# Optimization experiments

Measured on AMD Instinct MI355X. Metric: run time of the kernel, lower is better.

The kernel has to match this reference:

```python
import jax, jax.numpy as jnp
import numpy as np

N, E, D, B = 50000, 800000, 64, 64
NEXP, NC, EDIM, PDIM = 4, 10, 4, 100


def setup_inputs() -> dict:
    key = jax.random.key(0)
    ks = jax.random.split(key, 24)
    s = lambda f: 1.0 / np.sqrt(f)
    inp = {
        'x': jax.random.normal(ks[0], (N, D), jnp.float32),
        'edge_index': jax.random.randint(ks[1], (2, E), 0, N, jnp.int32),
        'edge_attr': jax.random.normal(ks[2], (E, EDIM), jnp.float32),
        'batch': jnp.sort(jax.random.randint(ks[3], (N,), 0, B, jnp.int32)),
        'ldxb_flag': jax.random.normal(ks[4], (B,), jnp.float32),
        # layer 1 params
        'w_edge1': jax.random.normal(ks[5], (D, EDIM)) * s(EDIM),
        'b_edge1': jnp.zeros((D,), jnp.float32),
        'w_ih1': jax.random.normal(ks[6], (3 * D, D)) * s(D),
        'w_hh1': jax.random.normal(ks[7], (3 * D, D)) * s(D),
        'b_ih1': jnp.zeros((3 * D,), jnp.float32),
        'b_hh1': jnp.zeros((3 * D,), jnp.float32),
        # layer 2 params
        'w_edge2': jax.random.normal(ks[8], (D, EDIM)) * s(EDIM),
        'b_edge2': jnp.zeros((D,), jnp.float32),
        'w_ih2': jax.random.normal(ks[9], (3 * D, D)) * s(D),
        'w_hh2': jax.random.normal(ks[10], (3 * D, D)) * s(D),
        'b_ih2': jnp.zeros((3 * D,), jnp.float32),
        'b_hh2': jnp.zeros((3 * D,), jnp.float32),
        # MoE
        'gate_w': jax.random.normal(ks[11], (NEXP, D)) * s(D),
        'gate_b': jnp.zeros((NEXP,), jnp.float32),
        'exp_w': jax.random.normal(ks[12], (NEXP, D, D)) * s(D),
        'exp_b': jnp.zeros((NEXP, D), jnp.float32),
        # heads
        'proj_w': jax.random.normal(ks[13], (PDIM, 1)),
        'proj_b': jnp.zeros((PDIM,), jnp.float32),
        'fc_w': jax.random.normal(ks[14], (NC, D + PDIM)) * s(D + PDIM),
        'fc_b': jnp.zeros((NC,), jnp.float32),
    }
    return inp


def _ggnn_layer(x, src, dst, eemb, w_ih, w_hh, b_ih, b_hh):
    # gather + scatter-add message passing (self-loops already in src/dst/eemb)
    msg = x[src] + eemb                       # [E+N, D]
    m = jnp.zeros_like(x).at[dst].add(msg)    # [N, D]
    # GRUCell(m, x): x is the hidden state
    gi = m @ w_ih.T + b_ih
    gh = x @ w_hh.T + b_hh
    i_r, i_z, i_n = jnp.split(gi, 3, axis=1)
    h_r, h_z, h_n = jnp.split(gh, 3, axis=1)
    r = jax.nn.sigmoid(i_r + h_r)
    z = jax.nn.sigmoid(i_z + h_z)
    n = jnp.tanh(i_n + r * h_n)
    return (1.0 - z) * n + z * x


def reference(x, edge_index, edge_attr, batch, ldxb_flag,
              w_edge1, b_edge1, w_ih1, w_hh1, b_ih1, b_hh1,
              w_edge2, b_edge2, w_ih2, w_hh2, b_ih2, b_hh2,
              gate_w, gate_b, exp_w, exp_b, proj_w, proj_b, fc_w, fc_b):
    n = x.shape[0]
    loop = jnp.arange(n, dtype=edge_index.dtype)
    src = jnp.concatenate([edge_index[0], loop])
    dst = jnp.concatenate([edge_index[1], loop])
    ea = jnp.concatenate([edge_attr, jnp.zeros((n, edge_attr.shape[1]), edge_attr.dtype)], axis=0)

    h = _ggnn_layer(x, src, dst, ea @ w_edge1.T + b_edge1, w_ih1, w_hh1, b_ih1, b_hh1)
    h = jax.nn.relu(h)
    h = _ggnn_layer(h, src, dst, ea @ w_edge2.T + b_edge2, w_ih2, w_hh2, b_ih2, b_hh2)
    h = jax.nn.relu(h)

    # soft MoE combine
    gw = jax.nn.softmax(h @ gate_w.T + gate_b, axis=1)            # [N, NEXP]
    eo = jax.nn.relu(jnp.einsum('nd,ehd->neh', h, exp_w) + exp_b)  # [N, NEXP, D]
    h = jnp.einsum('ne,neh->nh', gw, eo)                           # [N, D]

    # global mean pool per graph
    sums = jax.ops.segment_sum(h, batch, num_segments=B)
    cnts = jax.ops.segment_sum(jnp.ones((n,), h.dtype), batch, num_segments=B)
    graph_emb = sums / jnp.maximum(cnts, 1.0)[:, None]             # [B, D]

    flag = ldxb_flag[:, None] @ proj_w.T + proj_b                  # [B, 100]
    logits = jnp.concatenate([flag, graph_emb], axis=1) @ fc_w.T + fc_b
    return (graph_emb, graph_emb, logits)
```

## Files before the change

### kernel.cpp

```cpp
#include <hip/hip_runtime.h>
#include <stdint.h>


#define SUBCAP 6
#define OVF_MAX 32768
#define PS 16

typedef __bf16 bf16x8 __attribute__((ext_vector_type(8)));
typedef float floatx4 __attribute__((ext_vector_type(4)));
typedef unsigned short us8 __attribute__((ext_vector_type(8)));

__device__ __forceinline__ unsigned short f2bf(float f){
  union { float f; unsigned u; } c; c.f = f;
  unsigned r = c.u + 0x7FFFu + ((c.u >> 16) & 1u);
  return (unsigned short)(r >> 16);
}
__device__ __forceinline__ float bf2f(unsigned short u){
  union { unsigned u; float f; } c; c.u = ((unsigned)u) << 16; return c.f;
}
__device__ __forceinline__ float sigm(float x){ return 1.f/(1.f + __expf(-x)); }

__global__ void k_init(const float* __restrict__ s0, const float* __restrict__ s1,
                       const float* __restrict__ s2, const float* __restrict__ s3,
                       const float* __restrict__ s4, const float* __restrict__ s5,
                       unsigned short* __restrict__ dst,
                       int* __restrict__ cur, int* __restrict__ ovfcnt, int N8){
  int i = blockIdx.x*blockDim.x + threadIdx.x;
  if (i < N8) cur[i] = 0;
  if (i == 0){ ovfcnt[0] = 0; }
  if (i >= 65792) return;
  const float* s; int off;
  if      (i < 12288){ s = s0; off = i; }
  else if (i < 24576){ s = s1; off = i - 12288; }
  else if (i < 36864){ s = s2; off = i - 24576; }
  else if (i < 49152){ s = s3; off = i - 36864; }
  else if (i < 49408){ s = s4; off = i - 49152; }
  else               { s = s5; off = i - 49408; }
  dst[i] = f2bf(s[off]);
}

__global__ void k_bucket(const int* __restrict__ ei, const float* __restrict__ ea,
                         int* __restrict__ cur, int4* __restrict__ bkt,
                         int* __restrict__ ovfcnt, int* __restrict__ ovf,
                         int E, int N){
  int base = (blockIdx.x*blockDim.x + threadIdx.x)*2;
  if (base >= E) return;
  int sub = blockIdx.x & 7;
  bool v1 = base + 1 < E;
  int2 ss = *(const int2*)(ei + base);
  int2 dd = *(const int2*)(ei + E + base);
  if (!v1){ dd.y = dd.x; ss.y = ss.x; }
  float4 a0 = *(const float4*)(ea + (size_t)base*4);
  float4 a1 = v1 ? *(const float4*)(ea + (size_t)(base+1)*4) : a0;
  size_t sb0 = (size_t)sub*N + dd.x;
  size_t sb1 = (size_t)sub*N + dd.y;
  int p0 = atomicAdd(&cur[sb0], 1);
  int p1 = v1 ? atomicAdd(&cur[sb1], 1) : SUBCAP;
  if (p0 < SUBCAP){
    int4 rec;
    rec.x = ss.x;
    rec.y = (int)((unsigned)f2bf(a0.x) | ((unsigned)f2bf(a0.y) << 16));
    rec.z = (int)((unsigned)f2bf(a0.z) | ((unsigned)f2bf(a0.w) << 16));
    rec.w = 0;
    bkt[sb0*SUBCAP + p0] = rec;
  } else {
    int o = atomicAdd(ovfcnt, 1);
    if (o < OVF_MAX) ovf[o] = base;
  }
  if (v1){
    if (p1 < SUBCAP){
      int4 rec;
      rec.x = ss.y;
      rec.y = (int)((unsigned)f2bf(a1.x) | ((unsigned)f2bf(a1.y) << 16));
      rec.z = (int)((unsigned)f2bf(a1.z) | ((unsigned)f2bf(a1.w) << 16));
      rec.w = 0;
      bkt[sb1*SUBCAP + p1] = rec;
    } else {
      int o = atomicAdd(ovfcnt, 1);
      if (o < OVF_MAX) ovf[o] = base + 1;
    }
  }
}

__global__ void __launch_bounds__(256) k_gather(
    const int* __restrict__ cur, const int4* __restrict__ bkt,
    const float* __restrict__ xin,
    const float* __restrict__ w_edge, const float* __restrict__ b_edge,
    float* __restrict__ m, int N){
  int n = (int)(((long long)blockIdx.x*blockDim.x + threadIdx.x) >> 6);
  if (n >= N) return;
  int d = threadIdx.x & 63;
  int sub = d >> 3, k = d & 7;
  size_t sb = (size_t)sub*N + n;
  int myc = cur[sb];
  int contrib = (k == 0) ? myc : 0;
#pragma unroll
  for (int off = 1; off < 64; off <<= 1) contrib += __shfl_xor(contrib, off);
  int degAll = contrib;

  bool valid = k < min(myc, SUBCAP);
  int src = 0;
  float esx = 0.f, esy = 0.f, esz = 0.f, esw = 0.f;
  if (valid){
    int4 rec = bkt[sb*SUBCAP + k];
    src = rec.x;
    esx = bf2f((unsigned short)(rec.y      ));
    esy = bf2f((unsigned short)(rec.y >> 16));
    esz = bf2f((unsigned short)(rec.z      ));
    esw = bf2f((unsigned short)(rec.z >> 16));
  }

  float4 wv = *(const float4*)(w_edge + d*4);
  float acc = xin[(size_t)n*64 + d] + (float)(degAll + 1) * b_edge[d];

  unsigned long long mm = __ballot(valid);
  while (mm){
    int l0 = (int)__builtin_ctzll(mm); mm &= mm - 1;
    int s0 = __shfl(src, l0);
    float a0 = xin[(size_t)s0*64 + d];
    float a1 = 0.f, a2 = 0.f, a3 = 0.f;
    if (mm){
      int l1 = (int)__builtin_ctzll(mm); mm &= mm - 1;
      int s1 = __shfl(src, l1);
      a1 = xin[(size_t)s1*64 + d];
      if (mm){
        int l2 = (int)__builtin_ctzll(mm); mm &= mm - 1;
        int s2 = __shfl(src, l2);
        a2 = xin[(size_t)s2*64 + d];
        if (mm){
          int l3 = (int)__builtin_ctzll(mm); mm &= mm - 1;
          int s3 = __shfl(src, l3);
          a3 = xin[(size_t)s3*64 + d];
        }
      }
    }
    acc += (a0 + a1) + (a2 + a3);
  }

#pragma unroll
  for (int off = 1; off < 64; off <<= 1){
    esx += __shfl_xor(esx, off);
    esy += __shfl_xor(esy, off);
    esz += __shfl_xor(esz, off);
    esw += __shfl_xor(esw, off);
  }
  acc += esx*wv.x + esy*wv.y + esz*wv.z + esw*wv.w;
  m[(size_t)n*64 + d] = acc;
}

__global__ void k_ovf(const int* __restrict__ ei, const float* __restrict__ ea,
                      const float* __restrict__ xin, const float* __restrict__ w_edge,
                      const int* __restrict__ ovf, const int* __restrict__ ovfcnt,
                      float* __restrict__ m, int E){
  int cnt = *ovfcnt; if (cnt > OVF_MAX) cnt = OVF_MAX;
  int nwaves = (gridDim.x * blockDim.x) >> 6;
  int wid = (int)((blockIdx.x*blockDim.x + threadIdx.x) >> 6);
  int d = threadIdx.x & 63;
  for (int k = wid; k < cnt; k += nwaves){
    int e = ovf[k];
    int s = ei[e], dst = ei[E + e];
    float4 v  = *(const float4*)(ea + (size_t)e*4);
    float4 wv = *(const float4*)(w_edge + d*4);
    float msg = xin[(size_t)s*64 + d] + v.x*wv.x + v.y*wv.y + v.z*wv.z + v.w*wv.w;
    atomicAdd(&m[(size_t)dst*64 + d], msg);
  }
}

__global__ void __launch_bounds__(256) k_gru(
    const float* __restrict__ m, const float* x,
    const unsigned short* __restrict__ wih, const unsigned short* __restrict__ whh,
    const float* __restrict__ b_ih, const float* __restrict__ b_hh,
    float* out, int tiles, int N){
  int wid = (int)(((long long)blockIdx.x*blockDim.x + threadIdx.x) >> 6);
  if (wid >= tiles) return;
  int lane = threadIdx.x & 63;
  int col = lane & 15, quad = lane >> 4;
  int na = wid*16 + col; if (na > N-1) na = N-1;

  bf16x8 am[2], ax[2];
#pragma unroll
  for (int ks = 0; ks < 2; ++ks){
    int kb = ks*32 + quad*8;
    const float4* mp = (const float4*)(m + (size_t)na*64 + kb);
    float4 lo = mp[0], hi = mp[1];
    us8 tm;
    tm[0]=f2bf(lo.x); tm[1]=f2bf(lo.y); tm[2]=f2bf(lo.z); tm[3]=f2bf(lo.w);
    tm[4]=f2bf(hi.x); tm[5]=f2bf(hi.y); tm[6]=f2bf(hi.z); tm[7]=f2bf(hi.w);
    am[ks] = __builtin_bit_cast(bf16x8, tm);
    const float4* xp = (const float4*)(x + (size_t)na*64 + kb);
    float4 xlo = xp[0], xhi = xp[1];
    us8 tx;
    tx[0]=f2bf(xlo.x); tx[1]=f2bf(xlo.y); tx[2]=f2bf(xlo.z); tx[3]=f2bf(xlo.w);
    tx[4]=f2bf(xhi.x); tx[5]=f2bf(xhi.y); tx[6]=f2bf(xhi.z); tx[7]=f2bf(xhi.w);
    ax[ks] = __builtin_bit_cast(bf16x8, tx);
  }

  floatx4 ai[12], ah[12];
#pragma unroll
  for (int nt = 0; nt < 12; ++nt){ ai[nt] = (floatx4)0.f; ah[nt] = (floatx4)0.f; }
#pragma unroll
  for (int nt = 0; nt < 12; ++nt){
    int r = nt*16 + col;
#pragma unroll
    for (int ks = 0; ks < 2; ++ks){
      int kb = ks*32 + quad*8;
      bf16x8 bi = __builtin_bit_cast(bf16x8, *(const us8*)(wih + (size_t)r*64 + kb));
      ai[nt] = __builtin_amdgcn_mfma_f32_16x16x32_bf16(am[ks], bi, ai[nt], 0,0,0);
      bf16x8 bh = __builtin_bit_cast(bf16x8, *(const us8*)(whh + (size_t)r*64 + kb));
      ah[nt] = __builtin_amdgcn_mfma_f32_16x16x32_bf16(ax[ks], bh, ah[nt], 0,0,0);
    }
  }

#pragma unroll
  for (int nt = 0; nt < 4; ++nt){
    int d = nt*16 + col;
    float bir = b_ih[d],      bhr = b_hh[d];
    float biz = b_ih[64+d],   bhz = b_hh[64+d];
    float bin = b_ih[128+d],  bhn = b_hh[128+d];
#pragma unroll
    for (int rg = 0; rg < 4; ++rg){
      int node = wid*16 + quad*4 + rg;
      if (node >= N) continue;
      float rr = sigm(ai[nt  ][rg] + bir + ah[nt  ][rg] + bhr);
      float zz = sigm(ai[nt+4][rg] + biz + ah[nt+4][rg] + bhz);
      float nn = tanhf(ai[nt+8][rg] + bin + rr*(ah[nt+8][rg] + bhn));
      float xv = x[(size_t)node*64 + d];
      float hv = (1.f - zz)*nn + zz*xv;
      out[(size_t)node*64 + d] = fmaxf(hv, 0.f);
    }
  }
}

__global__ void __launch_bounds__(256) k_moe(
    const float* __restrict__ h,
    const unsigned short* __restrict__ gate_w, const float* __restrict__ gate_b,
    const unsigned short* __restrict__ exp_w,  const float* __restrict__ exp_b,
    float* __restrict__ v_out, int tiles, int N){
  __shared__ float gsm[4][16][4];
  int gwid = (int)(((long long)blockIdx.x*blockDim.x + threadIdx.x) >> 6);
  int w = threadIdx.x >> 6;
  int lane = threadIdx.x & 63;
  int col = lane & 15, quad = lane >> 4;
  bool active = gwid < tiles;

  floatx4 accg = (floatx4)0.f;
  floatx4 acce[4][4];
#pragma unroll
  for (int e=0;e<4;++e)
#pragma unroll
    for (int nt=0;nt<4;++nt) acce[e][nt] = (floatx4)0.f;

  if (active){
    int na = gwid*16 + col; if (na > N-1) na = N-1;
    bf16x8 a[2];
#pragma unroll
    for (int ks=0; ks<2; ++ks){
      int kb = ks*32 + quad*8;
      const float4* hp = (const float4*)(h + (size_t)na*64 + kb);
      float4 lo = hp[0], hi = hp[1];
      us8 th;
      th[0]=f2bf(lo.x); th[1]=f2bf(lo.y); th[2]=f2bf(lo.z); th[3]=f2bf(lo.w);
      th[4]=f2bf(hi.x); th[5]=f2bf(hi.y); th[6]=f2bf(hi.z); th[7]=f2bf(hi.w);
      a[ks] = __builtin_bit_cast(bf16x8, th);
      us8 braw = {0,0,0,0,0,0,0,0};
      if (col < 4) braw = *(const us8*)(gate_w + col*64 + kb);
      accg = __builtin_amdgcn_mfma_f32_16x16x32_bf16(a[ks], __builtin_bit_cast(bf16x8, braw), accg, 0,0,0);
    }
#pragma unroll
    for (int e=0;e<4;++e)
#pragma unroll
      for (int nt=0;nt<4;++nt)
#pragma unroll
        for (int ks=0;ks<2;++ks){
          int kb = ks*32 + quad*8;
          bf16x8 b = __builtin_bit_cast(bf16x8,
              *(const us8*)(exp_w + ((size_t)e*64 + nt*16 + col)*64 + kb));
          acce[e][nt] = __builtin_amdgcn_mfma_f32_16x16x32_bf16(a[ks], b, acce[e][nt], 0,0,0);
        }
    if (col < 4){
      float gb = gate_b[col];
#pragma unroll
      for (int rg=0;rg<4;++rg) gsm[w][quad*4+rg][col] = accg[rg] + gb;
    }
  }
  __syncthreads();
  if (!active) return;

#pragma unroll
  for (int rg=0; rg<4; ++rg){
    int nrow = quad*4 + rg;
    int node = gwid*16 + nrow;
    if (node >= N) continue;
    float g0=gsm[w][nrow][0], g1=gsm[w][nrow][1], g2=gsm[w][nrow][2], g3=gsm[w][nrow][3];
    float mx = fmaxf(fmaxf(g0,g1), fmaxf(g2,g3));
    float e0=__expf(g0-mx), e1=__expf(g1-mx), e2=__expf(g2-mx), e3=__expf(g3-mx);
    float inv = 1.f/(e0+e1+e2+e3);
    float w0=e0*inv, w1=e1*inv, w2=e2*inv, w3=e3*inv;
#pragma unroll
    for (int nt=0;nt<4;++nt){
      int o = nt*16 + col;
      float v = w0*fmaxf(acce[0][nt][rg] + exp_b[      o], 0.f)
              + w1*fmaxf(acce[1][nt][rg] + exp_b[ 64 + o], 0.f)
              + w2*fmaxf(acce[2][nt][rg] + exp_b[128 + o], 0.f)
              + w3*fmaxf(acce[3][nt][rg] + exp_b[192 + o], 0.f);
      v_out[(size_t)node*64 + o] = v;
    }
  }
}

__device__ __forceinline__ int lower_bound_i(const int* __restrict__ a, int n, int key){
  int lo = 0, hi = n;
  while (lo < hi){ int mid = (lo + hi) >> 1; if (a[mid] < key) lo = mid + 1; else hi = mid; }
  return lo;
}

__global__ void __launch_bounds__(256) k_pool(
    const float* __restrict__ v, const int* __restrict__ batch, int N,
    float* __restrict__ partial){
  __shared__ float red[4][64];
  int g = blockIdx.x / PS, s = blockIdx.x % PS;
  int t = threadIdx.x, d = t & 63, r = t >> 6;
  int start = lower_bound_i(batch, N, g);
  int end   = lower_bound_i(batch, N, g + 1);
  int len = end - start;
  int per = (len + PS - 1) / PS;
  int s0 = start + s*per;
  int s1 = s0 + per; if (s1 > end) s1 = end;
  float acc = 0.f;
  for (int i = s0 + r; i < s1; i += 4)
    acc += v[(size_t)i*64 + d];
  red[r][d] = acc;
  __syncthreads();
  if (r == 0)
    partial[(size_t)blockIdx.x*64 + d] = red[0][d] + red[1][d] + red[2][d] + red[3][d];
}

__global__ void __launch_bounds__(64) k_head(
    const float* __restrict__ partial, const int* __restrict__ batch, int N, int B,
    const float* __restrict__ ldxb,
    const float* __restrict__ proj_w, const float* __restrict__ proj_b,
    const float* __restrict__ fc_w, const float* __restrict__ fc_b,
    float* __restrict__ out){
  __shared__ float ges[64];
  int b = blockIdx.x, d = threadIdx.x;
  int start = lower_bound_i(batch, N, b);
  int end   = lower_bound_i(batch, N, b + 1);
  float sum = 0.f;
#pragma unroll
  for (int s = 0; s < PS; ++s)
    sum += partial[((size_t)b*PS + s)*64 + d];
  float ge = sum / fmaxf((float)(end - start), 1.f);
  ges[d] = ge;
  out[(size_t)b*64 + d]                = ge;
  out[(size_t)B*64 + (size_t)b*64 + d] = ge;
  __syncthreads();
  if (d < 10){
    float acc = fc_b[d];
    float fl = ldxb[b];
    const float* fr = fc_w + d*164;
    for (int p = 0; p < 100; ++p) acc += (fl*proj_w[p] + proj_b[p]) * fr[p];
    for (int dd = 0; dd < 64; ++dd) acc += ges[dd]*fr[100 + dd];
    out[(size_t)B*128 + (size_t)b*10 + d] = acc;
  }
}

extern "C" void kernel_launch(void* const* d_in, const int* in_sizes, int n_in,
                              void* d_out, int out_size, void* d_ws, size_t ws_size,
                              hipStream_t stream){
  const float* x      = (const float*)d_in[0];
  const int*   ei     = (const int*)d_in[1];
  const float* ea     = (const float*)d_in[2];
  const int*   batch  = (const int*)d_in[3];
  const float* ldxb   = (const float*)d_in[4];
  const float* w_edge1= (const float*)d_in[5];
  const float* b_edge1= (const float*)d_in[6];
  const float* w_ih1  = (const float*)d_in[7];
  const float* w_hh1  = (const float*)d_in[8];
  const float* b_ih1  = (const float*)d_in[9];
  const float* b_hh1  = (const float*)d_in[10];
  const float* w_edge2= (const float*)d_in[11];
  const float* b_edge2= (const float*)d_in[12];
  const float* w_ih2  = (const float*)d_in[13];
  const float* w_hh2  = (const float*)d_in[14];
  const float* b_ih2  = (const float*)d_in[15];
  const float* b_hh2  = (const float*)d_in[16];
  const float* gate_w = (const float*)d_in[17];
  const float* gate_b = (const float*)d_in[18];
  const float* exp_w  = (const float*)d_in[19];
  const float* exp_b  = (const float*)d_in[20];
  const float* proj_w = (const float*)d_in[21];
  const float* proj_b = (const float*)d_in[22];
  const float* fc_w   = (const float*)d_in[23];
  const float* fc_b   = (const float*)d_in[24];
  float* out = (float*)d_out;

  int N = in_sizes[0] / 64;
  int E = in_sizes[1] / 2;
  int B = in_sizes[4];
  int tiles = (N + 15) / 16;
  int nTot = N * 64;

  float*   m       = (float*)d_ws;
  float*   h       = m + (size_t)nTot;
  int4*    bkt     = (int4*)(h + (size_t)nTot);
  int*     cur     = (int*)(bkt + (size_t)N*8*SUBCAP);
  int*     ovfcnt  = cur + (size_t)N*8;
  int*     ovf     = ovfcnt + 4;
  unsigned short* wbf = (unsigned short*)(ovf + OVF_MAX);
  float*   partial = (float*)(wbf + 65792);
  unsigned short* wih1bf = wbf;
  unsigned short* whh1bf = wbf + 12288;
  unsigned short* wih2bf = wbf + 24576;
  unsigned short* whh2bf = wbf + 36864;
  unsigned short* gatebf = wbf + 49152;
  unsigned short* expbf  = wbf + 49408;

  dim3 blk(256);
  int edgePairBlocks = (((E + 1)/2) + 255)/256;
  int nodeWaveBlocks = (N + 3)/4;
  int waveBlocks = (tiles + 3)/4;
  int N8 = N*8;
  int initBlocks = ((N8 > 65792 ? N8 : 65792) + 255)/256;

  k_init<<<initBlocks, blk, 0, stream>>>(w_ih1, w_hh1, w_ih2, w_hh2, gate_w, exp_w,
                                         wbf, cur, ovfcnt, N8);
  k_bucket<<<edgePairBlocks, blk, 0, stream>>>(ei, ea, cur, bkt, ovfcnt, ovf, E, N);
  k_gather<<<nodeWaveBlocks, blk, 0, stream>>>(cur, bkt, x, w_edge1, b_edge1, m, N);
  k_ovf<<<64, blk, 0, stream>>>(ei, ea, x, w_edge1, ovf, ovfcnt, m, E);
  k_gru<<<waveBlocks, blk, 0, stream>>>(m, x, wih1bf, whh1bf, b_ih1, b_hh1, h, tiles, N);
  k_gather<<<nodeWaveBlocks, blk, 0, stream>>>(cur, bkt, h, w_edge2, b_edge2, m, N);
  k_ovf<<<64, blk, 0, stream>>>(ei, ea, h, w_edge2, ovf, ovfcnt, m, E);
  k_gru<<<waveBlocks, blk, 0, stream>>>(m, h, wih2bf, whh2bf, b_ih2, b_hh2, h, tiles, N);
  k_moe<<<waveBlocks, blk, 0, stream>>>(h, gatebf, gate_b, expbf, exp_b, m, tiles, N);
  k_pool<<<B*PS, blk, 0, stream>>>(m, batch, N, partial);
  k_head<<<B, 64, 0, stream>>>(partial, batch, N, B, ldxb, proj_w, proj_b, fc_w, fc_b, out);
}
```

Before: 385.6 us.

## Keep bf16 shadow copies of node features for gather, GRU and MoE

Node features are converted to bf16 once: in the init kernel for x, and as an extra output of the GRU kernel for h. The gather, GRU and MoE kernels then read these bf16 copies instead of fp32, halving the bytes moved by the random neighbour gathers and removing repeated fp32-to-bf16 conversions. The bucket sub-capacity also rises from 6 to 8 so all eight lanes per sub-bucket can hold edges, sending fewer edges to the atomic overflow path. In exchange, neighbour messages are summed from bf16-rounded features, which costs some accuracy, and there is an extra bf16 write per layer plus a larger bucket array.

```diff
diff --git a/kernel.cpp b/kernel.cpp
--- a/kernel.cpp
+++ b/kernel.cpp
@@ -2,7 +2,7 @@
 #include <stdint.h>
 
 
-#define SUBCAP 6
+#define SUBCAP 8
 #define OVF_MAX 32768
 #define PS 16
 
@@ -20,12 +20,15 @@
 }
 __device__ __forceinline__ float sigm(float x){ return 1.f/(1.f + __expf(-x)); }
 
-__global__ void k_init(const float* __restrict__ s0, const float* __restrict__ s1,
+__global__ void k_init(const float* __restrict__ x, unsigned short* __restrict__ x_bf,
+                       const float* __restrict__ s0, const float* __restrict__ s1,
                        const float* __restrict__ s2, const float* __restrict__ s3,
                        const float* __restrict__ s4, const float* __restrict__ s5,
                        unsigned short* __restrict__ dst,
-                       int* __restrict__ cur, int* __restrict__ ovfcnt, int N8){
+                       int* __restrict__ cur, int* __restrict__ ovfcnt,
+                       int nTot, int N8){
   int i = blockIdx.x*blockDim.x + threadIdx.x;
+  if (i < nTot) x_bf[i] = f2bf(x[i]);
   if (i < N8) cur[i] = 0;
   if (i == 0){ ovfcnt[0] = 0; }
   if (i >= 65792) return;
@@ -84,7 +87,7 @@
 
 __global__ void __launch_bounds__(256) k_gather(
     const int* __restrict__ cur, const int4* __restrict__ bkt,
-    const float* __restrict__ xin,
+    const unsigned short* __restrict__ xbf,
     const float* __restrict__ w_edge, const float* __restrict__ b_edge,
     float* __restrict__ m, int N){
   int n = (int)(((long long)blockIdx.x*blockDim.x + threadIdx.x) >> 6);
@@ -111,26 +114,26 @@
   }
 
   float4 wv = *(const float4*)(w_edge + d*4);
-  float acc = xin[(size_t)n*64 + d] + (float)(degAll + 1) * b_edge[d];
+  float acc = bf2f(xbf[(size_t)n*64 + d]) + (float)(degAll + 1) * b_edge[d];
 
   unsigned long long mm = __ballot(valid);
   while (mm){
     int l0 = (int)__builtin_ctzll(mm); mm &= mm - 1;
     int s0 = __shfl(src, l0);
-    float a0 = xin[(size_t)s0*64 + d];
+    float a0 = bf2f(xbf[(size_t)s0*64 + d]);
     float a1 = 0.f, a2 = 0.f, a3 = 0.f;
     if (mm){
       int l1 = (int)__builtin_ctzll(mm); mm &= mm - 1;
       int s1 = __shfl(src, l1);
-      a1 = xin[(size_t)s1*64 + d];
+      a1 = bf2f(xbf[(size_t)s1*64 + d]);
       if (mm){
         int l2 = (int)__builtin_ctzll(mm); mm &= mm - 1;
         int s2 = __shfl(src, l2);
-        a2 = xin[(size_t)s2*64 + d];
+        a2 = bf2f(xbf[(size_t)s2*64 + d]);
         if (mm){
           int l3 = (int)__builtin_ctzll(mm); mm &= mm - 1;
           int s3 = __shfl(src, l3);
-          a3 = xin[(size_t)s3*64 + d];
+          a3 = bf2f(xbf[(size_t)s3*64 + d]);
         }
       }
     }
@@ -168,9 +171,10 @@
 
 __global__ void __launch_bounds__(256) k_gru(
     const float* __restrict__ m, const float* x,
+    const unsigned short* __restrict__ xbf,
     const unsigned short* __restrict__ wih, const unsigned short* __restrict__ whh,
     const float* __restrict__ b_ih, const float* __restrict__ b_hh,
-    float* out, int tiles, int N){
+    float* out, unsigned short* out_bf, int tiles, int N){
   int wid = (int)(((long long)blockIdx.x*blockDim.x + threadIdx.x) >> 6);
   if (wid >= tiles) return;
   int lane = threadIdx.x & 63;
@@ -187,12 +191,7 @@
     tm[0]=f2bf(lo.x); tm[1]=f2bf(lo.y); tm[2]=f2bf(lo.z); tm[3]=f2bf(lo.w);
     tm[4]=f2bf(hi.x); tm[5]=f2bf(hi.y); tm[6]=f2bf(hi.z); tm[7]=f2bf(hi.w);
     am[ks] = __builtin_bit_cast(bf16x8, tm);
-    const float4* xp = (const float4*)(x + (size_t)na*64 + kb);
-    float4 xlo = xp[0], xhi = xp[1];
-    us8 tx;
-    tx[0]=f2bf(xlo.x); tx[1]=f2bf(xlo.y); tx[2]=f2bf(xlo.z); tx[3]=f2bf(xlo.w);
-    tx[4]=f2bf(xhi.x); tx[5]=f2bf(xhi.y); tx[6]=f2bf(xhi.z); tx[7]=f2bf(xhi.w);
-    ax[ks] = __builtin_bit_cast(bf16x8, tx);
+    ax[ks] = __builtin_bit_cast(bf16x8, *(const us8*)(xbf + (size_t)na*64 + kb));
   }
 
   floatx4 ai[12], ah[12];
@@ -225,14 +224,15 @@
       float zz = sigm(ai[nt+4][rg] + biz + ah[nt+4][rg] + bhz);
       float nn = tanhf(ai[nt+8][rg] + bin + rr*(ah[nt+8][rg] + bhn));
       float xv = x[(size_t)node*64 + d];
-      float hv = (1.f - zz)*nn + zz*xv;
-      out[(size_t)node*64 + d] = fmaxf(hv, 0.f);
+      float hv = fmaxf((1.f - zz)*nn + zz*xv, 0.f);
+      out[(size_t)node*64 + d] = hv;
+      out_bf[(size_t)node*64 + d] = f2bf(hv);
     }
   }
 }
 
 __global__ void __launch_bounds__(256) k_moe(
-    const float* __restrict__ h,
+    const unsigned short* __restrict__ hbf,
     const unsigned short* __restrict__ gate_w, const float* __restrict__ gate_b,
     const unsigned short* __restrict__ exp_w,  const float* __restrict__ exp_b,
     float* __restrict__ v_out, int tiles, int N){
@@ -256,12 +256,7 @@
 #pragma unroll
     for (int ks=0; ks<2; ++ks){
       int kb = ks*32 + quad*8;
-      const float4* hp = (const float4*)(h + (size_t)na*64 + kb);
-      float4 lo = hp[0], hi = hp[1];
-      us8 th;
-      th[0]=f2bf(lo.x); th[1]=f2bf(lo.y); th[2]=f2bf(lo.z); th[3]=f2bf(lo.w);
-      th[4]=f2bf(hi.x); th[5]=f2bf(hi.y); th[6]=f2bf(hi.z); th[7]=f2bf(hi.w);
-      a[ks] = __builtin_bit_cast(bf16x8, th);
+      a[ks] = __builtin_bit_cast(bf16x8, *(const us8*)(hbf + (size_t)na*64 + kb));
       us8 braw = {0,0,0,0,0,0,0,0};
       if (col < 4) braw = *(const us8*)(gate_w + col*64 + kb);
       accg = __builtin_amdgcn_mfma_f32_16x16x32_bf16(a[ks], __builtin_bit_cast(bf16x8, braw), accg, 0,0,0);
@@ -402,7 +397,9 @@
 
   float*   m       = (float*)d_ws;
   float*   h       = m + (size_t)nTot;
-  int4*    bkt     = (int4*)(h + (size_t)nTot);
+  unsigned short* x_bf = (unsigned short*)(h + (size_t)nTot);
+  unsigned short* h_bf = x_bf + (size_t)nTot;
+  int4*    bkt     = (int4*)(h_bf + (size_t)nTot);
   int*     cur     = (int*)(bkt + (size_t)N*8*SUBCAP);
   int*     ovfcnt  = cur + (size_t)N*8;
   int*     ovf     = ovfcnt + 4;
@@ -420,18 +417,21 @@
   int nodeWaveBlocks = (N + 3)/4;
   int waveBlocks = (tiles + 3)/4;
   int N8 = N*8;
-  int initBlocks = ((N8 > 65792 ? N8 : 65792) + 255)/256;
-
-  k_init<<<initBlocks, blk, 0, stream>>>(w_ih1, w_hh1, w_ih2, w_hh2, gate_w, exp_w,
-                                         wbf, cur, ovfcnt, N8);
+  int initMax = nTot > N8 ? nTot : N8; if (initMax < 65792) initMax = 65792;
+  int initBlocks = (initMax + 255)/256;
+
+  k_init<<<initBlocks, blk, 0, stream>>>(x, x_bf, w_ih1, w_hh1, w_ih2, w_hh2,
+                                         gate_w, exp_w, wbf, cur, ovfcnt, nTot, N8);
   k_bucket<<<edgePairBlocks, blk, 0, stream>>>(ei, ea, cur, bkt, ovfcnt, ovf, E, N);
-  k_gather<<<nodeWaveBlocks, blk, 0, stream>>>(cur, bkt, x, w_edge1, b_edge1, m, N);
+  k_gather<<<nodeWaveBlocks, blk, 0, stream>>>(cur, bkt, x_bf, w_edge1, b_edge1, m, N);
   k_ovf<<<64, blk, 0, stream>>>(ei, ea, x, w_edge1, ovf, ovfcnt, m, E);
-  k_gru<<<waveBlocks, blk, 0, stream>>>(m, x, wih1bf, whh1bf, b_ih1, b_hh1, h, tiles, N);
-  k_gather<<<nodeWaveBlocks, blk, 0, stream>>>(cur, bkt, h, w_edge2, b_edge2, m, N);
+  k_gru<<<waveBlocks, blk, 0, stream>>>(m, x, x_bf, wih1bf, whh1bf, b_ih1, b_hh1,
+                                        h, h_bf, tiles, N);
+  k_gather<<<nodeWaveBlocks, blk, 0, stream>>>(cur, bkt, h_bf, w_edge2, b_edge2, m, N);
   k_ovf<<<64, blk, 0, stream>>>(ei, ea, h, w_edge2, ovf, ovfcnt, m, E);
-  k_gru<<<waveBlocks, blk, 0, stream>>>(m, h, wih2bf, whh2bf, b_ih2, b_hh2, h, tiles, N);
-  k_moe<<<waveBlocks, blk, 0, stream>>>(h, gatebf, gate_b, expbf, exp_b, m, tiles, N);
+  k_gru<<<waveBlocks, blk, 0, stream>>>(m, h, h_bf, wih2bf, whh2bf, b_ih2, b_hh2,
+                                        h, h_bf, tiles, N);
+  k_moe<<<waveBlocks, blk, 0, stream>>>(h_bf, gatebf, gate_b, expbf, exp_b, m, tiles, N);
   k_pool<<<B*PS, blk, 0, stream>>>(m, batch, N, partial);
   k_head<<<B, 64, 0, stream>>>(partial, batch, N, B, ldxb, proj_w, proj_b, fc_w, fc_b, out);
 }
```

Measured after the change: 369.2 us. 1.04x faster.
